# Kernel tuning notes

Hardware: AMD Instinct MI355X
Metric: run time of the kernel (lower is better)

The kernel has to match this reference:

```python
import jax, jax.numpy as jnp
import numpy as np

B, S, HID = 1, 4096, 768
NH, HD = 12, 64  # num heads, head dim


def setup_inputs() -> dict:
    key = jax.random.key(0)
    ks = jax.random.split(key, 7)
    scale = 1.0 / np.sqrt(HID)
    return {
        "hidden_states": jax.random.normal(ks[0], (B, S, HID), dtype=jnp.float32),
        "attention_mask": jnp.zeros((B, 1, 1, S), dtype=jnp.float32),
        "Wq": jax.random.normal(ks[1], (HID, HID), dtype=jnp.float32) * scale,
        "bq": jnp.zeros((HID,), dtype=jnp.float32),
        "Wk": jax.random.normal(ks[2], (HID, HID), dtype=jnp.float32) * scale,
        "bk": jnp.zeros((HID,), dtype=jnp.float32),
        "Wv": jax.random.normal(ks[3], (HID, HID), dtype=jnp.float32) * scale,
        "bv": jnp.zeros((HID,), dtype=jnp.float32),
    }


def _split_heads(x):
    # [B,S,HID] -> [B,NH,S,HD]
    b, s, _ = x.shape
    return x.reshape(b, s, NH, HD).transpose(0, 2, 1, 3)


def reference(hidden_states, attention_mask, Wq, bq, Wk, bk, Wv, bv):
    q = _split_heads(jnp.einsum('bsh,ho->bso', hidden_states, Wq) + bq)
    k = _split_heads(jnp.einsum('bsh,ho->bso', hidden_states, Wk) + bk)
    v = _split_heads(jnp.einsum('bsh,ho->bso', hidden_states, Wv) + bv)
    # attention scores: [B,NH,S,S]
    scores = jnp.einsum('bnqd,bnkd->bnqk', q, k) / np.sqrt(HD)
    scores = scores + attention_mask  # additive mask broadcast [B,1,1,S]
    probs = jax.nn.softmax(scores, axis=-1)
    ctx = jnp.einsum('bnqk,bnkd->bnqd', probs, v)
    # [B,NH,S,HD] -> [B,S,HID]
    b = ctx.shape[0]
    return ctx.transpose(0, 2, 1, 3).reshape(b, -1, NH * HD)
```

## Files before the change

kernel.cpp:

```cpp
#include <hip/hip_runtime.h>

typedef _Float16 f16;
typedef __attribute__((ext_vector_type(8))) _Float16 half8;
typedef __attribute__((ext_vector_type(4))) _Float16 half4;
typedef __attribute__((ext_vector_type(4))) float f32x4;

#define S_LEN 4096
#define HID   768
#define NH    12
#define HD    64

#define EXP2(x) __builtin_amdgcn_exp2f(x)

__global__ __launch_bounds__(256) void k_convert_x(const float* __restrict__ x,
                                                   f16* __restrict__ xb) {
  int i = blockIdx.x * 256 + threadIdx.x;
  float4 v = ((const float4*)x)[i];
  half4 h;
  h[0] = (f16)v.x; h[1] = (f16)v.y; h[2] = (f16)v.z; h[3] = (f16)v.w;
  *(half4*)&xb[(size_t)i * 4] = h;
}

__global__ __launch_bounds__(256) void k_transw(const float* __restrict__ Wq,
                                                const float* __restrict__ Wk,
                                                const float* __restrict__ Wv,
                                                f16* __restrict__ wtb) {
  __shared__ float tile[32][33];
  const float* W = (blockIdx.z == 0) ? Wq : (blockIdx.z == 1 ? Wk : Wv);
  f16* wt = wtb + (size_t)blockIdx.z * HID * HID;
  int k0 = blockIdx.y * 32, n0 = blockIdx.x * 32;
  int tx = threadIdx.x, ty = threadIdx.y;
  #pragma unroll
  for (int j = ty; j < 32; j += 8)
    tile[j][tx] = W[(size_t)(k0 + j) * HID + n0 + tx];
  __syncthreads();
  #pragma unroll
  for (int j = ty; j < 32; j += 8)
    wt[(size_t)(n0 + j) * HID + k0 + tx] = (f16)tile[tx][j];
}

__global__ __launch_bounds__(256) void k_gemm_qkv(const f16* __restrict__ xb,
                                                  const f16* __restrict__ wtb,
                                                  const float* __restrict__ bq,
                                                  const float* __restrict__ bk,
                                                  const float* __restrict__ bv,
                                                  f16* __restrict__ qo,
                                                  f16* __restrict__ ko,
                                                  f16* __restrict__ vto) {
  __shared__ __align__(16) f16 As[128 * 32];
  __shared__ __align__(16) f16 Bs[128 * 32];
  const int z = blockIdx.z;
  const f16* wt = wtb + (size_t)z * HID * HID;
  const float* bias = (z == 0) ? bq : (z == 1 ? bk : bv);
  const int brow = blockIdx.y * 128;
  const int bcol = blockIdx.x * 128;
  const int tid = threadIdx.x, wid = tid >> 6, lane = tid & 63;
  const int wr = wid >> 1, wc = wid & 1;
  const int lrow = lane & 15, lk8 = (lane >> 4) * 8;
  const int srow = lane >> 2;
  const int scol = (lane & 3) * 8;

  f32x4 acc[4][4] = {};

  for (int kt = 0; kt < HID; kt += 32) {
    #pragma unroll
    for (int r = 0; r < 2; r++) {
      int row = (wid * 2 + r) * 16 + srow;
      const f16* ga = xb + (size_t)(brow + row) * HID + kt + scol;
      const f16* gb = wt + (size_t)(bcol + row) * HID + kt + scol;
      __builtin_amdgcn_global_load_lds(
          (const __attribute__((address_space(1))) void*)ga,
          (__attribute__((address_space(3))) void*)(As + (wid * 2 + r) * 512),
          16, 0, 0);
      __builtin_amdgcn_global_load_lds(
          (const __attribute__((address_space(1))) void*)gb,
          (__attribute__((address_space(3))) void*)(Bs + (wid * 2 + r) * 512),
          16, 0, 0);
    }
    __syncthreads();

    half8 a[4], b[4];
    #pragma unroll
    for (int m = 0; m < 4; m++)
      a[m] = *(const half8*)&As[(wr * 64 + m * 16 + lrow) * 32 + lk8];
    #pragma unroll
    for (int n = 0; n < 4; n++)
      b[n] = *(const half8*)&Bs[(wc * 64 + n * 16 + lrow) * 32 + lk8];
    #pragma unroll
    for (int m = 0; m < 4; m++)
      #pragma unroll
      for (int n = 0; n < 4; n++)
        acc[m][n] = __builtin_amdgcn_mfma_f32_16x16x32_f16(a[m], b[n], acc[m][n], 0, 0, 0);
    __syncthreads();
  }

  #pragma unroll
  for (int m = 0; m < 4; m++) {
    int row0 = brow + wr * 64 + m * 16 + (lane >> 4) * 4;
    #pragma unroll
    for (int n = 0; n < 4; n++) {
      int col = bcol + wc * 64 + n * 16 + lrow;
      float bsv = bias[col];
      int h = col >> 6, d = col & 63;
      #pragma unroll
      for (int i = 0; i < 4; i++) {
        f16 v = (f16)(acc[m][n][i] + bsv);
        int r2 = row0 + i;
        if (z == 2)      vto[(size_t)(h * HD + d) * S_LEN + r2] = v;
        else if (z == 1) ko[((size_t)h * S_LEN + r2) * HD + d] = v;
        else             qo[((size_t)h * S_LEN + r2) * HD + d] = v;
      }
    }
  }
}

__global__ __launch_bounds__(256) void k_attn(const f16* __restrict__ qb,
                                              const f16* __restrict__ kb,
                                              const f16* __restrict__ vt,
                                              const float* __restrict__ mask,
                                              float* __restrict__ out) {
  __shared__ __align__(16) f16 Ks[2][64 * 64];
  __shared__ __align__(16) f16 Vs[2][64 * 64];
  __shared__ __align__(16) f16 P[4][16 * 72];
  const int h = blockIdx.y;
  const int tid = threadIdx.x, wid = tid >> 6, lane = tid & 63;
  const int lrow = lane & 15, lk8 = (lane >> 4) * 8, g4 = (lane >> 4) * 4;
  const int grp = lane >> 4;
  const int qrow0 = blockIdx.x * 64 + wid * 16;
  const size_t hqk = (size_t)h * (S_LEN * HD);
  f16* Pw = &P[wid][0];
  const float LOG2E = 1.4426950408889634f;
  const float scale2 = 0.125f * LOG2E;

  const int srow = tid >> 3;
  const int sc   = tid & 7;

  const half8 aq0 = *(const half8*)&qb[hqk + (size_t)(qrow0 + lrow) * HD + lk8];
  const half8 aq1 = *(const half8*)&qb[hqk + (size_t)(qrow0 + lrow) * HD + 32 + lk8];

  f32x4 acc[4] = {};
  float mi = -INFINITY, li = 0.f;

  auto stage = [&](int buf, int kt) {
    #pragma unroll
    for (int r = 0; r < 2; r++) {
      const int row = r * 32 + srow;
      const int scol = ((sc ^ (row & 7)) << 3);
      const f16* gk = kb + hqk + (size_t)(kt + row) * HD + scol;
      const f16* gv = vt + ((size_t)(h * HD + row)) * S_LEN + kt + scol;
      f16* dk = &Ks[buf][r * 2048 + (tid << 3)];
      f16* dv = &Vs[buf][r * 2048 + (tid << 3)];
      __builtin_amdgcn_global_load_lds(
          (const __attribute__((address_space(1))) void*)gk,
          (__attribute__((address_space(3))) void*)dk, 16, 0, 0);
      __builtin_amdgcn_global_load_lds(
          (const __attribute__((address_space(1))) void*)gv,
          (__attribute__((address_space(3))) void*)dv, 16, 0, 0);
    }
  };

  stage(0, 0);
  __syncthreads();

  for (int it = 0; it < S_LEN / 64; ++it) {
    const int cur = it & 1;
    const int kt = it * 64;
    if (it + 1 < S_LEN / 64) stage(cur ^ 1, kt + 64);

    f32x4 sp[4];
    #pragma unroll
    for (int nt = 0; nt < 4; nt++) {
      const int row = nt * 16 + lrow;
      const int x0 = ((grp ^ (row & 7)) << 3);
      const int x1 = (((4 + grp) ^ (row & 7)) << 3);
      half8 b0 = *(const half8*)&Ks[cur][row * 64 + x0];
      half8 b1 = *(const half8*)&Ks[cur][row * 64 + x1];
      f32x4 sv = {};
      sv = __builtin_amdgcn_mfma_f32_16x16x32_f16(b0, aq0, sv, 0, 0, 0);
      sv = __builtin_amdgcn_mfma_f32_16x16x32_f16(b1, aq1, sv, 0, 0, 0);
      sp[nt] = sv;
    }
    float mloc = -INFINITY;
    #pragma unroll
    for (int nt = 0; nt < 4; nt++) {
      float4 mk = *(const float4*)&mask[kt + nt * 16 + g4];
      sp[nt][0] = sp[nt][0] * scale2 + mk.x * LOG2E;
      sp[nt][1] = sp[nt][1] * scale2 + mk.y * LOG2E;
      sp[nt][2] = sp[nt][2] * scale2 + mk.z * LOG2E;
      sp[nt][3] = sp[nt][3] * scale2 + mk.w * LOG2E;
      mloc = fmaxf(mloc, fmaxf(fmaxf(sp[nt][0], sp[nt][1]), fmaxf(sp[nt][2], sp[nt][3])));
    }
    mloc = fmaxf(mloc, __shfl_xor(mloc, 16, 64));
    mloc = fmaxf(mloc, __shfl_xor(mloc, 32, 64));
    const float mn = fmaxf(mi, mloc);
    const float al = EXP2(mi - mn);
    mi = mn;
    float rs = 0.f;
    #pragma unroll
    for (int nt = 0; nt < 4; nt++)
      #pragma unroll
      for (int i = 0; i < 4; i++) {
        sp[nt][i] = EXP2(sp[nt][i] - mn);
        rs += sp[nt][i];
      }
    rs += __shfl_xor(rs, 16, 64);
    rs += __shfl_xor(rs, 32, 64);
    li = li * al + rs;
    #pragma unroll
    for (int nd = 0; nd < 4; nd++) {
      acc[nd][0] *= al; acc[nd][1] *= al; acc[nd][2] *= al; acc[nd][3] *= al;
    }
    #pragma unroll
    for (int nt = 0; nt < 4; nt++) {
      half4 h4;
      h4[0] = (f16)sp[nt][0]; h4[1] = (f16)sp[nt][1];
      h4[2] = (f16)sp[nt][2]; h4[3] = (f16)sp[nt][3];
      *(half4*)&Pw[lrow * 72 + nt * 16 + g4] = h4;
    }
    #pragma unroll
    for (int k2 = 0; k2 < 2; k2++) {
      half8 bp = *(const half8*)&Pw[lrow * 72 + k2 * 32 + lk8];
      #pragma unroll
      for (int nd = 0; nd < 4; nd++) {
        const int vr = nd * 16 + lrow;
        const int xc = (((k2 * 4 + grp) ^ (vr & 7)) << 3);
        half8 av = *(const half8*)&Vs[cur][vr * 64 + xc];
        acc[nd] = __builtin_amdgcn_mfma_f32_16x16x32_f16(av, bp, acc[nd], 0, 0, 0);
      }
    }
    __syncthreads();
  }

  const float inv = (li > 0.f) ? (1.f / li) : 0.f;
  #pragma unroll
  for (int nd = 0; nd < 4; nd++) {
    float4 o = make_float4(acc[nd][0] * inv, acc[nd][1] * inv,
                           acc[nd][2] * inv, acc[nd][3] * inv);
    *(float4*)&out[(size_t)(qrow0 + lrow) * HID + h * HD + nd * 16 + g4] = o;
  }
}

extern "C" void kernel_launch(void* const* d_in, const int* in_sizes, int n_in,
                              void* d_out, int out_size, void* d_ws, size_t ws_size,
                              hipStream_t stream) {
  const float* x    = (const float*)d_in[0];
  const float* mask = (const float*)d_in[1];
  const float* Wq   = (const float*)d_in[2];
  const float* bq   = (const float*)d_in[3];
  const float* Wk   = (const float*)d_in[4];
  const float* bk   = (const float*)d_in[5];
  const float* Wv   = (const float*)d_in[6];
  const float* bv   = (const float*)d_in[7];
  float* out = (float*)d_out;

  char* ws = (char*)d_ws;
  f16* xb  = (f16*)(ws);
  f16* wtb = (f16*)(ws + 6291456);
  f16* qbb = (f16*)(ws + 9830400);
  f16* kbb = (f16*)(ws + 16121856);
  f16* vtb = (f16*)(ws + 22413312);

  k_convert_x<<<dim3(3072), dim3(256), 0, stream>>>(x, xb);
  k_transw<<<dim3(24, 24, 3), dim3(32, 8), 0, stream>>>(Wq, Wk, Wv, wtb);
  k_gemm_qkv<<<dim3(6, 32, 3), dim3(256), 0, stream>>>(xb, wtb, bq, bk, bv, qbb, kbb, vtb);
  k_attn<<<dim3(64, NH), dim3(256), 0, stream>>>(qbb, kbb, vtb, mask, out);
}
```

Before: 166.8 us.

## Skip lazy softmax rescale, premultiply mask, batch K loads, prioritize MFMA

Several attention-loop tweaks. The running max and accumulator rescale are now updated only when some lane's new max exceeds the old one by more than 8, which removes most of the per-tile exp2 and multiply work. The mask is pre-scaled by log2(e) in a new small kernel that reuses the dead xb workspace region. K fragment loads are batched ahead of the MFMAs, s_setprio is raised around the MFMA blocks, and the probabilities are packed to fp16 with cvt_pkrtz. The lazy rescale lets probabilities reach 2^8 in fp16, and round-toward-zero conversion slightly changes numerics.

```diff
diff --git a/kernel.cpp b/kernel.cpp
--- a/kernel.cpp
+++ b/kernel.cpp
@@ -3,6 +3,7 @@
 typedef _Float16 f16;
 typedef __attribute__((ext_vector_type(8))) _Float16 half8;
 typedef __attribute__((ext_vector_type(4))) _Float16 half4;
+typedef __attribute__((ext_vector_type(2))) _Float16 half2v;
 typedef __attribute__((ext_vector_type(4))) float f32x4;
 
 #define S_LEN 4096
@@ -11,6 +12,7 @@
 #define HD    64
 
 #define EXP2(x) __builtin_amdgcn_exp2f(x)
+#define PKRTZ(a, b) __builtin_bit_cast(half2v, __builtin_amdgcn_cvt_pkrtz((a), (b)))
 
 __global__ __launch_bounds__(256) void k_convert_x(const float* __restrict__ x,
                                                    f16* __restrict__ xb) {
@@ -19,6 +21,14 @@
   half4 h;
   h[0] = (f16)v.x; h[1] = (f16)v.y; h[2] = (f16)v.z; h[3] = (f16)v.w;
   *(half4*)&xb[(size_t)i * 4] = h;
+}
+
+__global__ __launch_bounds__(256) void k_maskcvt(const float* __restrict__ m,
+                                                 float* __restrict__ m2) {
+  int i = blockIdx.x * 256 + threadIdx.x;
+  const float LOG2E = 1.4426950408889634f;
+  float4 v = ((const float4*)m)[i];
+  ((float4*)m2)[i] = make_float4(v.x * LOG2E, v.y * LOG2E, v.z * LOG2E, v.w * LOG2E);
 }
 
 __global__ __launch_bounds__(256) void k_transw(const float* __restrict__ Wq,
@@ -117,7 +127,7 @@
 __global__ __launch_bounds__(256) void k_attn(const f16* __restrict__ qb,
                                               const f16* __restrict__ kb,
                                               const f16* __restrict__ vt,
-                                              const float* __restrict__ mask,
+                                              const float* __restrict__ mask2,
                                               float* __restrict__ out) {
   __shared__ __align__(16) f16 Ks[2][64 * 64];
   __shared__ __align__(16) f16 Vs[2][64 * 64];
@@ -168,58 +178,77 @@
     if (it + 1 < S_LEN / 64) stage(cur ^ 1, kt + 64);
 
     f32x4 sp[4];
+    {
+      half8 b0[4], b1[4];
+      #pragma unroll
+      for (int nt = 0; nt < 4; nt++) {
+        const int row = nt * 16 + lrow;
+        b0[nt] = *(const half8*)&Ks[cur][row * 64 + ((grp ^ (row & 7)) << 3)];
+        b1[nt] = *(const half8*)&Ks[cur][row * 64 + (((4 + grp) ^ (row & 7)) << 3)];
+      }
+      __builtin_amdgcn_s_setprio(1);
+      #pragma unroll
+      for (int nt = 0; nt < 4; nt++) {
+        f32x4 sv = {};
+        sv = __builtin_amdgcn_mfma_f32_16x16x32_f16(b0[nt], aq0, sv, 0, 0, 0);
+        sv = __builtin_amdgcn_mfma_f32_16x16x32_f16(b1[nt], aq1, sv, 0, 0, 0);
+        sp[nt] = sv;
+      }
+      __builtin_amdgcn_s_setprio(0);
+    }
     #pragma unroll
     for (int nt = 0; nt < 4; nt++) {
-      const int row = nt * 16 + lrow;
-      const int x0 = ((grp ^ (row & 7)) << 3);
-      const int x1 = (((4 + grp) ^ (row & 7)) << 3);
-      half8 b0 = *(const half8*)&Ks[cur][row * 64 + x0];
-      half8 b1 = *(const half8*)&Ks[cur][row * 64 + x1];
-      f32x4 sv = {};
-      sv = __builtin_amdgcn_mfma_f32_16x16x32_f16(b0, aq0, sv, 0, 0, 0);
-      sv = __builtin_amdgcn_mfma_f32_16x16x32_f16(b1, aq1, sv, 0, 0, 0);
-      sp[nt] = sv;
-    }
-    float mloc = -INFINITY;
-    #pragma unroll
-    for (int nt = 0; nt < 4; nt++) {
-      float4 mk = *(const float4*)&mask[kt + nt * 16 + g4];
-      sp[nt][0] = sp[nt][0] * scale2 + mk.x * LOG2E;
-      sp[nt][1] = sp[nt][1] * scale2 + mk.y * LOG2E;
-      sp[nt][2] = sp[nt][2] * scale2 + mk.z * LOG2E;
-      sp[nt][3] = sp[nt][3] * scale2 + mk.w * LOG2E;
-      mloc = fmaxf(mloc, fmaxf(fmaxf(sp[nt][0], sp[nt][1]), fmaxf(sp[nt][2], sp[nt][3])));
-    }
+      float4 mk = *(const float4*)&mask2[kt + nt * 16 + g4];
+      sp[nt][0] = sp[nt][0] * scale2 + mk.x;
+      sp[nt][1] = sp[nt][1] * scale2 + mk.y;
+      sp[nt][2] = sp[nt][2] * scale2 + mk.z;
+      sp[nt][3] = sp[nt][3] * scale2 + mk.w;
+    }
+    float mloc = fmaxf(sp[0][0], sp[0][1]);
+    mloc = fmaxf(fmaxf(mloc, sp[0][2]), sp[0][3]);
+    mloc = fmaxf(fmaxf(mloc, sp[1][0]), sp[1][1]);
+    mloc = fmaxf(fmaxf(mloc, sp[1][2]), sp[1][3]);
+    mloc = fmaxf(fmaxf(mloc, sp[2][0]), sp[2][1]);
+    mloc = fmaxf(fmaxf(mloc, sp[2][2]), sp[2][3]);
+    mloc = fmaxf(fmaxf(mloc, sp[3][0]), sp[3][1]);
+    mloc = fmaxf(fmaxf(mloc, sp[3][2]), sp[3][3]);
     mloc = fmaxf(mloc, __shfl_xor(mloc, 16, 64));
     mloc = fmaxf(mloc, __shfl_xor(mloc, 32, 64));
-    const float mn = fmaxf(mi, mloc);
-    const float al = EXP2(mi - mn);
-    mi = mn;
+
+    float al = 1.f;
+    if (!__all(mloc <= mi + 8.f)) {
+      const float mn = fmaxf(mi, mloc);
+      al = EXP2(mi - mn);
+      mi = mn;
+      #pragma unroll
+      for (int nd = 0; nd < 4; nd++) {
+        acc[nd][0] *= al; acc[nd][1] *= al; acc[nd][2] *= al; acc[nd][3] *= al;
+      }
+    }
     float rs = 0.f;
     #pragma unroll
     for (int nt = 0; nt < 4; nt++)
       #pragma unroll
       for (int i = 0; i < 4; i++) {
-        sp[nt][i] = EXP2(sp[nt][i] - mn);
+        sp[nt][i] = EXP2(sp[nt][i] - mi);
         rs += sp[nt][i];
       }
     rs += __shfl_xor(rs, 16, 64);
     rs += __shfl_xor(rs, 32, 64);
     li = li * al + rs;
-    #pragma unroll
-    for (int nd = 0; nd < 4; nd++) {
-      acc[nd][0] *= al; acc[nd][1] *= al; acc[nd][2] *= al; acc[nd][3] *= al;
-    }
+
     #pragma unroll
     for (int nt = 0; nt < 4; nt++) {
+      half2v lo = PKRTZ(sp[nt][0], sp[nt][1]);
+      half2v hi = PKRTZ(sp[nt][2], sp[nt][3]);
       half4 h4;
-      h4[0] = (f16)sp[nt][0]; h4[1] = (f16)sp[nt][1];
-      h4[2] = (f16)sp[nt][2]; h4[3] = (f16)sp[nt][3];
+      h4[0] = lo[0]; h4[1] = lo[1]; h4[2] = hi[0]; h4[3] = hi[1];
       *(half4*)&Pw[lrow * 72 + nt * 16 + g4] = h4;
     }
     #pragma unroll
     for (int k2 = 0; k2 < 2; k2++) {
       half8 bp = *(const half8*)&Pw[lrow * 72 + k2 * 32 + lk8];
+      __builtin_amdgcn_s_setprio(1);
       #pragma unroll
       for (int nd = 0; nd < 4; nd++) {
         const int vr = nd * 16 + lrow;
@@ -227,6 +256,7 @@
         half8 av = *(const half8*)&Vs[cur][vr * 64 + xc];
         acc[nd] = __builtin_amdgcn_mfma_f32_16x16x32_f16(av, bp, acc[nd], 0, 0, 0);
       }
+      __builtin_amdgcn_s_setprio(0);
     }
     __syncthreads();
   }
@@ -259,9 +289,11 @@
   f16* qbb = (f16*)(ws + 9830400);
   f16* kbb = (f16*)(ws + 16121856);
   f16* vtb = (f16*)(ws + 22413312);
+  float* mask2 = (float*)ws;
 
   k_convert_x<<<dim3(3072), dim3(256), 0, stream>>>(x, xb);
   k_transw<<<dim3(24, 24, 3), dim3(32, 8), 0, stream>>>(Wq, Wk, Wv, wtb);
   k_gemm_qkv<<<dim3(6, 32, 3), dim3(256), 0, stream>>>(xb, wtb, bq, bk, bv, qbb, kbb, vtb);
-  k_attn<<<dim3(64, NH), dim3(256), 0, stream>>>(qbb, kbb, vtb, mask, out);
-}
+  k_maskcvt<<<dim3(4), dim3(256), 0, stream>>>(mask, mask2);
+  k_attn<<<dim3(64, NH), dim3(256), 0, stream>>>(qbb, kbb, vtb, mask2, out);
+}
```

After: 149.2 us. 1.12x faster.
